# Kernel tuning notes

Measured on AMD Instinct MI355X. Metric: run time of the kernel, lower is better.

Reference implementation:

```python
import jax, jax.numpy as jnp
import numpy as np

TOP_K = 10  # hardcoded k in the original tf.math.top_k call
EPS = 1e-8


def _make_boxes(key, n):
    # valid xyxy boxes in a ~1024x1024 image
    k1, k2 = jax.random.split(key)
    xy = jax.random.uniform(k1, (n, 2), dtype=jnp.float32) * 900.0
    wh = jax.random.uniform(k2, (n, 2), dtype=jnp.float32) * 120.0 + 4.0
    return jnp.concatenate([xy, xy + wh], axis=-1)


def _pairwise_iou(a, b):
    # a: [N,4] xyxy, b: [M,4] xyxy -> [N,M]
    lt = jnp.maximum(a[:, None, :2], b[None, :, :2])  # [N,M,2]
    rb = jnp.minimum(a[:, None, 2:], b[None, :, 2:])  # [N,M,2]
    wh = jnp.clip(rb - lt, 0.0)
    inter = wh[..., 0] * wh[..., 1]                    # [N,M]
    area_a = (a[:, 2] - a[:, 0]) * (a[:, 3] - a[:, 1])  # [N]
    area_b = (b[:, 2] - b[:, 0]) * (b[:, 3] - b[:, 1])  # [M]
    union = area_a[:, None] + area_b[None, :] - inter
    return inter / (union + EPS)


def setup_inputs() -> dict:
    key = jax.random.key(0)
    k1, k2, k3, k4 = jax.random.split(key, 4)
    N, M, C = 16384, 2048, 81
    proposals = _make_boxes(k1, N)
    gt_proposals = _make_boxes(k2, M)
    cls_prob = jax.random.uniform(k3, (N, C), dtype=jnp.float32)
    gt_cls = jax.random.randint(k4, (M,), 0, C, dtype=jnp.int32)
    return {"proposals": proposals, "cls_prob": cls_prob,
            "gt_proposals": gt_proposals, "gt_cls": gt_cls}


def reference(proposals, cls_prob, gt_proposals, gt_cls):
    # Reachable math of ProposalTargetLayer.call (the original aborts via
    # embed()/exit() right after building the top-k mask `i`).
    iou = _pairwise_iou(proposals, gt_proposals)          # [N,M]
    flat = jnp.reshape(iou, (-1,))
    _, top_idx = jax.lax.top_k(flat, TOP_K)
    # tensor_scatter_nd_update of ones onto a zero tensor -> boolean top-k mask
    mask_flat = jnp.zeros_like(flat).at[top_idx].set(1.0)
    mask = jnp.reshape(mask_flat, iou.shape).astype(jnp.bool_)  # [N,M]
    return (iou, mask)
```

## Files before the change

kernel.cpp:

```cpp
#include <hip/hip_runtime.h>

#define TOPK 10
#define BLK 256
#define ROWS_PER_BLOCK 8
#define CAND_CAP 32768
#define SLACK 2e-5f
#define NSLOTS 10

typedef float f4vec __attribute__((ext_vector_type(4)));

__device__ __forceinline__ bool better(float v1, int i1, float v2, int i2) {
    return (v1 > v2) || (v1 == v2 && i1 < i2);
}

__device__ __forceinline__ void insert10(float (&lv)[TOPK], int (&li)[TOPK],
                                         float v, int ix, float& mv, int& mi) {
    int ws = 0; float wv = lv[0]; int wi = li[0];
#pragma unroll
    for (int j = 1; j < TOPK; ++j)
        if (better(wv, wi, lv[j], li[j])) { wv = lv[j]; wi = li[j]; ws = j; }
#pragma unroll
    for (int j = 0; j < TOPK; ++j)
        if (j == ws) { lv[j] = v; li[j] = ix; }
    mv = lv[0]; mi = li[0];
#pragma unroll
    for (int j = 1; j < TOPK; ++j)
        if (better(mv, mi, lv[j], li[j])) { mv = lv[j]; mi = li[j]; }
}

__device__ __forceinline__ void waveReduceTop10(float (&lv)[TOPK], int (&li)[TOPK],
                                                float* wcv, int* wci, int tid) {
    const int wave = tid >> 6;
    const int lane = tid & 63;
    for (int r = 0; r < TOPK; ++r) {
        float bv = lv[0]; int bi = li[0];
#pragma unroll
        for (int j = 1; j < TOPK; ++j)
            if (better(lv[j], li[j], bv, bi)) { bv = lv[j]; bi = li[j]; }
#pragma unroll
        for (int off = 32; off >= 1; off >>= 1) {
            float ov = __shfl_xor(bv, off, 64);
            int   oi = __shfl_xor(bi, off, 64);
            if (better(ov, oi, bv, bi)) { bv = ov; bi = oi; }
        }
#pragma unroll
        for (int j = 0; j < TOPK; ++j)
            if (lv[j] == bv && li[j] == bi) { lv[j] = -2.0f; li[j] = 0x7fffffff; }
        if (lane == 0) { wcv[wave * TOPK + r] = bv; wci[wave * TOPK + r] = bi; }
    }
}

template <typename EmitFn>
__device__ __forceinline__ void wave0FinalTop10(const float* wcv, const int* wci,
                                                int tid, EmitFn emit) {
    float v = (tid < 40) ? wcv[tid] : -2.0f;
    int   ix = (tid < 40) ? wci[tid] : 0x7fffffff;
    for (int r = 0; r < TOPK; ++r) {
        float bv = v; int bi = ix;
#pragma unroll
        for (int off = 32; off >= 1; off >>= 1) {
            float ov = __shfl_xor(bv, off, 64);
            int   oi = __shfl_xor(bi, off, 64);
            if (better(ov, oi, bv, bi)) { bv = ov; bi = oi; }
        }
        if (v == bv && ix == bi) { v = -2.0f; ix = 0x7fffffff; }
        if (tid == 0) emit(r, bv, bi);
    }
}

__device__ __forceinline__ float iou_exact(const float4 a, const float aA,
                                           const float4 b, const float bA) {
    const float ltx = fmaxf(a.x, b.x);
    const float lty = fmaxf(a.y, b.y);
    const float rbx = fminf(a.z, b.z);
    const float rby = fminf(a.w, b.w);
    const float w = fmaxf(rbx - ltx, 0.0f);
    const float h = fmaxf(rby - lty, 0.0f);
    const float inter = __fmul_rn(w, h);
    const float s = aA + bA;
    const float uni = s - inter;
    const float den = uni + 1e-8f;
    return inter / den;
}

__device__ __forceinline__ float iou_fast(const float4 a, const float aA,
                                          const float4 b, const float bA) {
    const float ltx = fmaxf(a.x, b.x);
    const float lty = fmaxf(a.y, b.y);
    const float rbx = fminf(a.z, b.z);
    const float rby = fminf(a.w, b.w);
    const float w = fmaxf(rbx - ltx, 0.0f);
    const float h = fmaxf(rby - lty, 0.0f);
    const float inter = w * h;
    const float den = (aA + bA - inter) + 1e-8f;
    return inter * __builtin_amdgcn_rcpf(den);
}

__global__ __launch_bounds__(BLK) void sample_max_kernel(
    const float4* __restrict__ prop, const float4* __restrict__ gt,
    unsigned int* __restrict__ slots, int N, int M) {
    const int tid = threadIdx.x;
    const int bid = blockIdx.x;
    const int row = bid * ROWS_PER_BLOCK + (tid & 7);
    long long c = ((long long)(tid >> 3) * M) >> 5;
    const int col = (int)((c + (bid & 63)) % M);

    float v = 0.0f;
    if (row < N) {
        const float4 a = prop[row];
        const float aA = (a.z - a.x) * (a.w - a.y);
        const float4 b = gt[col];
        const float bA = (b.z - b.x) * (b.w - b.y);
        v = iou_fast(a, aA, b, bA);
    }

    __shared__ float sred[4];
#pragma unroll
    for (int off = 32; off >= 1; off >>= 1)
        v = fmaxf(v, __shfl_xor(v, off, 64));
    if ((tid & 63) == 0) sred[tid >> 6] = v;
    __syncthreads();
    if (tid == 0) {
        const float bm = fmaxf(fmaxf(sred[0], sred[1]), fmaxf(sred[2], sred[3]));
        atomicMax(&slots[bid % NSLOTS], __float_as_uint(bm));
    }
}

__global__ __launch_bounds__(BLK) void iou_main_kernel(
    const float4* __restrict__ prop, const float4* __restrict__ gt,
    float* __restrict__ iou_out, float* __restrict__ mask_out,
    const unsigned int* __restrict__ slots, int* __restrict__ cand_cnt,
    int* __restrict__ cand_idx, int N, int M) {
    const int tid = threadIdx.x;
    const int bid = blockIdx.x;
    const int row0 = bid * ROWS_PER_BLOCK;

    unsigned int mn = slots[0];
#pragma unroll
    for (int s = 1; s < NSLOTS; ++s) mn = min(mn, slots[s]);
    const float Tm = __uint_as_float(mn) - SLACK;

    float4 pa[ROWS_PER_BLOCK];
    float  paA[ROWS_PER_BLOCK];
#pragma unroll
    for (int nl = 0; nl < ROWS_PER_BLOCK; ++nl) {
        const int r = row0 + nl;
        const float4 a = (r < N) ? prop[r] : make_float4(0.f, 0.f, 0.f, 0.f);
        pa[nl] = a;
        paA[nl] = (a.z - a.x) * (a.w - a.y);
    }

    const f4vec zero4 = {0.0f, 0.0f, 0.0f, 0.0f};
    for (int m0 = 4 * tid; m0 < M; m0 += 4 * BLK) {
        const float4 b0 = gt[m0 + 0], b1 = gt[m0 + 1], b2 = gt[m0 + 2], b3 = gt[m0 + 3];
        const float bA0 = (b0.z - b0.x) * (b0.w - b0.y);
        const float bA1 = (b1.z - b1.x) * (b1.w - b1.y);
        const float bA2 = (b2.z - b2.x) * (b2.w - b2.y);
        const float bA3 = (b3.z - b3.x) * (b3.w - b3.y);
#pragma unroll
        for (int nl = 0; nl < ROWS_PER_BLOCK; ++nl) {
            const int row = row0 + nl;
            if (row < N) {
                const float i0 = iou_fast(pa[nl], paA[nl], b0, bA0);
                const float i1 = iou_fast(pa[nl], paA[nl], b1, bA1);
                const float i2 = iou_fast(pa[nl], paA[nl], b2, bA2);
                const float i3 = iou_fast(pa[nl], paA[nl], b3, bA3);
                const long long base = (long long)row * M + m0;
                const f4vec iv = {i0, i1, i2, i3};
                *reinterpret_cast<f4vec*>(iou_out + base) = iv;
                *reinterpret_cast<f4vec*>(mask_out + base) = zero4;
                const float mx = fmaxf(fmaxf(i0, i1), fmaxf(i2, i3));
                if (mx >= Tm) {
                    if (i0 >= Tm) { int s = atomicAdd(cand_cnt, 1); if (s < CAND_CAP) cand_idx[s] = (int)base; }
                    if (i1 >= Tm) { int s = atomicAdd(cand_cnt, 1); if (s < CAND_CAP) cand_idx[s] = (int)base + 1; }
                    if (i2 >= Tm) { int s = atomicAdd(cand_cnt, 1); if (s < CAND_CAP) cand_idx[s] = (int)base + 2; }
                    if (i3 >= Tm) { int s = atomicAdd(cand_cnt, 1); if (s < CAND_CAP) cand_idx[s] = (int)base + 3; }
                }
            }
        }
    }
}

__global__ __launch_bounds__(BLK) void final_kernel(
    const float4* __restrict__ prop, const float4* __restrict__ gt,
    const int* __restrict__ cand_cnt, const int* __restrict__ cand_idx,
    float* __restrict__ mask_out, int M) {
    __shared__ float wcv[4 * TOPK];
    __shared__ int   wci[4 * TOPK];
    const int tid = threadIdx.x;
    int c = *cand_cnt;
    if (c > CAND_CAP) c = CAND_CAP;

    float lv[TOPK]; int li[TOPK];
#pragma unroll
    for (int j = 0; j < TOPK; ++j) { lv[j] = -2.0f; li[j] = 0x7fffffff; }
    float mv = -2.0f; int mi = 0x7fffffff;

    for (int i = tid; i < c; i += BLK) {
        const int idx = cand_idx[i];
        const int row = idx / M;
        const int col = idx - row * M;
        const float4 a = prop[row];
        const float4 b = gt[col];
        const float aA = __fmul_rn(a.z - a.x, a.w - a.y);
        const float bA = __fmul_rn(b.z - b.x, b.w - b.y);
        const float v = iou_exact(a, aA, b, bA);
        if (better(v, idx, mv, mi)) insert10(lv, li, v, idx, mv, mi);
    }
    waveReduceTop10(lv, li, wcv, wci, tid);
    __syncthreads();
    if (tid < 64) {
        wave0FinalTop10(wcv, wci, tid, [&](int r, float bv, int bi) {
            (void)r;
            if (bi >= 0 && bi != 0x7fffffff && bv >= 0.0f) mask_out[bi] = 1.0f;
        });
    }
}

extern "C" void kernel_launch(void* const* d_in, const int* in_sizes, int n_in,
                              void* d_out, int out_size, void* d_ws, size_t ws_size,
                              hipStream_t stream) {
    const float4* prop = (const float4*)d_in[0];
    const float4* gt = (const float4*)d_in[2];
    const int N = in_sizes[0] / 4;
    const int M = in_sizes[2] / 4;

    float* iou_out = (float*)d_out;
    float* mask_out = iou_out + (long long)N * M;

    char* ws = (char*)d_ws;
    unsigned int* slots = (unsigned int*)ws;
    int* cand_cnt = (int*)(ws + 40);
    int* cand_idx = (int*)(ws + 64);

    hipMemsetAsync(ws, 0, 44, stream);

    const int nblocks = (N + ROWS_PER_BLOCK - 1) / ROWS_PER_BLOCK;

    sample_max_kernel<<<nblocks, BLK, 0, stream>>>(prop, gt, slots, N, M);
    iou_main_kernel<<<nblocks, BLK, 0, stream>>>(prop, gt, iou_out, mask_out,
                                                 slots, cand_cnt, cand_idx, N, M);
    final_kernel<<<1, BLK, 0, stream>>>(prop, gt, cand_cnt, cand_idx, mask_out, M);
}
```

Before: 104.3 us.

## Fuse final top-k selection into main IoU kernel via last-block ticket

Folds the single-block final top-k kernel into the tail of the main IoU kernel: each block takes a ticket with an atomic counter after a threadfence, and only the last block to finish runs the candidate selection and writes the mask. This removes one kernel launch and its serialization gap. It also drops the per-row register cache of proposals, reloading each row's box inside the loop, and adds launch_bounds occupancy hints. The tail of M not divisible by 4 is no longer processed, and the final reduction now runs while other blocks may still be resident.

Result: slower. 372.1 us (+256.6%).

```diff
diff --git a/kernel.cpp b/kernel.cpp
--- a/kernel.cpp
+++ b/kernel.cpp
@@ -126,11 +126,12 @@
     }
 }
 
-__global__ __launch_bounds__(BLK) void iou_main_kernel(
+__global__ __launch_bounds__(BLK, 4) void iou_main_fused(
     const float4* __restrict__ prop, const float4* __restrict__ gt,
     float* __restrict__ iou_out, float* __restrict__ mask_out,
     const unsigned int* __restrict__ slots, int* __restrict__ cand_cnt,
-    int* __restrict__ cand_idx, int N, int M) {
+    int* __restrict__ cand_idx, unsigned int* __restrict__ done_cnt,
+    int N, int M, int nblocks) {
     const int tid = threadIdx.x;
     const int bid = blockIdx.x;
     const int row0 = bid * ROWS_PER_BLOCK;
@@ -140,18 +141,10 @@
     for (int s = 1; s < NSLOTS; ++s) mn = min(mn, slots[s]);
     const float Tm = __uint_as_float(mn) - SLACK;
 
-    float4 pa[ROWS_PER_BLOCK];
-    float  paA[ROWS_PER_BLOCK];
-#pragma unroll
-    for (int nl = 0; nl < ROWS_PER_BLOCK; ++nl) {
-        const int r = row0 + nl;
-        const float4 a = (r < N) ? prop[r] : make_float4(0.f, 0.f, 0.f, 0.f);
-        pa[nl] = a;
-        paA[nl] = (a.z - a.x) * (a.w - a.y);
-    }
-
+    const int M4 = M & ~3;
     const f4vec zero4 = {0.0f, 0.0f, 0.0f, 0.0f};
-    for (int m0 = 4 * tid; m0 < M; m0 += 4 * BLK) {
+
+    for (int m0 = 4 * tid; m0 < M4; m0 += 4 * BLK) {
         const float4 b0 = gt[m0 + 0], b1 = gt[m0 + 1], b2 = gt[m0 + 2], b3 = gt[m0 + 3];
         const float bA0 = (b0.z - b0.x) * (b0.w - b0.y);
         const float bA1 = (b1.z - b1.x) * (b1.w - b1.y);
@@ -161,16 +154,17 @@
         for (int nl = 0; nl < ROWS_PER_BLOCK; ++nl) {
             const int row = row0 + nl;
             if (row < N) {
-                const float i0 = iou_fast(pa[nl], paA[nl], b0, bA0);
-                const float i1 = iou_fast(pa[nl], paA[nl], b1, bA1);
-                const float i2 = iou_fast(pa[nl], paA[nl], b2, bA2);
-                const float i3 = iou_fast(pa[nl], paA[nl], b3, bA3);
+                const float4 a = prop[row];
+                const float aA = (a.z - a.x) * (a.w - a.y);
+                const float i0 = iou_fast(a, aA, b0, bA0);
+                const float i1 = iou_fast(a, aA, b1, bA1);
+                const float i2 = iou_fast(a, aA, b2, bA2);
+                const float i3 = iou_fast(a, aA, b3, bA3);
                 const long long base = (long long)row * M + m0;
                 const f4vec iv = {i0, i1, i2, i3};
                 *reinterpret_cast<f4vec*>(iou_out + base) = iv;
                 *reinterpret_cast<f4vec*>(mask_out + base) = zero4;
-                const float mx = fmaxf(fmaxf(i0, i1), fmaxf(i2, i3));
-                if (mx >= Tm) {
+                if (i0 >= Tm || i1 >= Tm || i2 >= Tm || i3 >= Tm) {
                     if (i0 >= Tm) { int s = atomicAdd(cand_cnt, 1); if (s < CAND_CAP) cand_idx[s] = (int)base; }
                     if (i1 >= Tm) { int s = atomicAdd(cand_cnt, 1); if (s < CAND_CAP) cand_idx[s] = (int)base + 1; }
                     if (i2 >= Tm) { int s = atomicAdd(cand_cnt, 1); if (s < CAND_CAP) cand_idx[s] = (int)base + 2; }
@@ -179,16 +173,19 @@
             }
         }
     }
-}
-
-__global__ __launch_bounds__(BLK) void final_kernel(
-    const float4* __restrict__ prop, const float4* __restrict__ gt,
-    const int* __restrict__ cand_cnt, const int* __restrict__ cand_idx,
-    float* __restrict__ mask_out, int M) {
+
     __shared__ float wcv[4 * TOPK];
     __shared__ int   wci[4 * TOPK];
-    const int tid = threadIdx.x;
-    int c = *cand_cnt;
+    __shared__ unsigned int s_ticket;
+
+    __syncthreads();
+    __threadfence();
+    if (tid == 0) s_ticket = atomicAdd(done_cnt, 1u);
+    __syncthreads();
+    if (s_ticket != (unsigned int)(nblocks - 1)) return;
+    __threadfence();
+
+    int c = atomicAdd(cand_cnt, 0);
     if (c > CAND_CAP) c = CAND_CAP;
 
     float lv[TOPK]; int li[TOPK];
@@ -197,7 +194,7 @@
     float mv = -2.0f; int mi = 0x7fffffff;
 
     for (int i = tid; i < c; i += BLK) {
-        const int idx = cand_idx[i];
+        const int idx = atomicAdd(&cand_idx[i], 0);
         const int row = idx / M;
         const int col = idx - row * M;
         const float4 a = prop[row];
@@ -228,17 +225,18 @@
     float* iou_out = (float*)d_out;
     float* mask_out = iou_out + (long long)N * M;
 
+    const int nblocks = (N + ROWS_PER_BLOCK - 1) / ROWS_PER_BLOCK;
+
     char* ws = (char*)d_ws;
     unsigned int* slots = (unsigned int*)ws;
     int* cand_cnt = (int*)(ws + 40);
+    unsigned int* done_cnt = (unsigned int*)(ws + 44);
     int* cand_idx = (int*)(ws + 64);
 
-    hipMemsetAsync(ws, 0, 44, stream);
-
-    const int nblocks = (N + ROWS_PER_BLOCK - 1) / ROWS_PER_BLOCK;
+    hipMemsetAsync(ws, 0, 48, stream);
 
     sample_max_kernel<<<nblocks, BLK, 0, stream>>>(prop, gt, slots, N, M);
-    iou_main_kernel<<<nblocks, BLK, 0, stream>>>(prop, gt, iou_out, mask_out,
-                                                 slots, cand_cnt, cand_idx, N, M);
-    final_kernel<<<1, BLK, 0, stream>>>(prop, gt, cand_cnt, cand_idx, mask_out, M);
-}
+    iou_main_fused<<<nblocks, BLK, 0, stream>>>(prop, gt, iou_out, mask_out,
+                                                slots, cand_cnt, cand_idx,
+                                                done_cnt, N, M, nblocks);
+}
```
